# Kernel tuning notes

Measured on AMD Instinct MI355X. Metric: run time of the kernel, lower is better.

Reference implementation:

```python
import jax, jax.numpy as jnp
import numpy as np

T, B, E, H = 1024, 4, 1024, 16


def setup_inputs() -> dict:
    key0 = jax.random.key(0)
    ks = jax.random.split(key0, 10)
    query = jax.random.normal(ks[0], (T, B, E), jnp.float32)
    key_t = jax.random.normal(ks[1], (T, B, E), jnp.float32)
    # causal additive mask [T, T] (0 on/below diagonal, -inf above)
    causal = jnp.where(jnp.tril(jnp.ones((T, T), bool)), 0.0, -jnp.inf).astype(jnp.float32)
    # per-row valid lengths in [T//2, T]; True = padded key position
    lengths = jax.random.randint(ks[2], (B,), T // 2, T + 1)
    key_padding_mask = jnp.arange(T)[None, :] >= lengths[:, None]  # [B, T] bool
    scale = E ** -0.5
    Wq = jax.random.normal(ks[3], (E, E), jnp.float32) * scale
    Wk = jax.random.normal(ks[4], (E, E), jnp.float32) * scale
    Wv = jax.random.normal(ks[5], (E, E), jnp.float32) * scale
    bq = jax.random.normal(ks[6], (E,), jnp.float32) * 0.02
    bk = jax.random.normal(ks[7], (E,), jnp.float32) * 0.02
    bv = jax.random.normal(ks[8], (E,), jnp.float32) * 0.02
    return dict(query=query, key=key_t, key_padding_mask=key_padding_mask,
                attn_mask=causal, Wq=Wq, bq=bq, Wk=Wk, bk=bk, Wv=Wv, bv=bv,
                num_heads=H)


def reference(query, key, key_padding_mask, attn_mask, Wq, bq, Wk, bk, Wv, bv, num_heads):
    # Self-attention path (encoder_decoder_attention=False, layer_state=None):
    # k, v computed from `query`; `key` is unused (matches torch forward).
    t, b, e = query.shape
    h = num_heads
    d = e // h
    scaling = d ** -0.5
    q = (query @ Wq.T + bq) * scaling          # [T, B, E]
    k = query @ Wk.T + bk
    v = query @ Wv.T + bv

    def _shape(x):  # [T, B, E] -> [B*H, T, D]
        return x.reshape(t, b * h, d).transpose(1, 0, 2)

    q, k, v = _shape(q), _shape(k), _shape(v)
    attn = jnp.einsum('ztd,zsd->zts', q, k)    # [B*H, T, S]
    attn = attn.reshape(b, h, t, t) + attn_mask            # additive causal mask
    attn = jnp.where(key_padding_mask[:, None, None, :], -jnp.inf, attn)
    probs = jax.nn.softmax(attn, axis=-1)                   # dropout p=0.0
    out = jnp.einsum('bhts,bhsd->bhtd', probs, v.reshape(b, h, t, d))
    # [B,H,T,D] -> [B*H,T,D] -> [T,B*H,D] -> [T,B,E]
    out = out.reshape(b * h, t, d).transpose(1, 0, 2).reshape(t, b, e)
    return out
```

## Files before the change

kernel.cpp:

```cpp
#include <hip/hip_runtime.h>
#include <cstdint>


typedef __attribute__((ext_vector_type(8))) short short8;
typedef __attribute__((ext_vector_type(4))) float floatx4;
typedef __attribute__((ext_vector_type(16))) float floatx16;
typedef __attribute__((ext_vector_type(4))) unsigned short u16x4;
typedef unsigned short u16;

#define T_DIM 1024
#define B_DIM 4
#define E_DIM 1024
#define H_DIM 16
#define D_DIM 64
#define M_DIM (T_DIM * B_DIM)
#define N_DIM (3 * E_DIM)
#define K_DIM E_DIM
#define KT_NUM (K_DIM / 64)

__device__ __forceinline__ u16 f2bf(float f) {
  uint32_t u = __builtin_bit_cast(uint32_t, f);
  u += 0x7fffu + ((u >> 16) & 1u);
  return (u16)(u >> 16);
}

__device__ __forceinline__ void gload_lds16(const void* g, void* l) {
  __builtin_amdgcn_global_load_lds(
      (const __attribute__((address_space(1))) uint32_t*)g,
      (__attribute__((address_space(3))) uint32_t*)l, 16, 0, 0);
}

__device__ __forceinline__ uint32_t swz(uint32_t row, uint32_t cb) {
  return row * 128u + (cb ^ ((row & 7u) << 4));
}

#define BARRIER()  __builtin_amdgcn_s_barrier()
#define WAIT_VM6   asm volatile("s_waitcnt vmcnt(6)" ::: "memory")
#define WAIT_VM0   asm volatile("s_waitcnt vmcnt(0)" ::: "memory")

__global__ __launch_bounds__(256) void convert_k(
    const float* __restrict__ q, const float* __restrict__ wq,
    const float* __restrict__ wk, const float* __restrict__ wv,
    u16* __restrict__ Abf, u16* __restrict__ Wbf,
    const int* __restrict__ kpm, int* __restrict__ lengths) {
  if (blockIdx.x >= 7168) {
    __shared__ int cnt;
    if (threadIdx.x == 0) cnt = 0;
    __syncthreads();
    int b = blockIdx.x - 7168;
    int local = 0;
    for (int t = threadIdx.x; t < T_DIM; t += 256)
      local += (kpm[b * T_DIM + t] == 0) ? 1 : 0;
    atomicAdd(&cnt, local);
    __syncthreads();
    if (threadIdx.x == 0) lengths[b] = cnt;
    return;
  }
  size_t i = ((size_t)blockIdx.x * 256 + threadIdx.x) * 4;
  const float* src;
  u16* dst;
  if (i < (size_t)M_DIM * K_DIM) {
    src = q + i;
    dst = Abf + i;
  } else {
    size_t off = i - (size_t)M_DIM * K_DIM;
    int x = (int)(off >> 20);
    size_t within = off & 1048575u;
    src = (x == 0 ? wq : (x == 1 ? wk : wv)) + within;
    dst = Wbf + off;
  }
  float4 v = *(const float4*)src;
  u16x4 o;
  o.x = f2bf(v.x); o.y = f2bf(v.y); o.z = f2bf(v.z); o.w = f2bf(v.w);
  *(u16x4*)dst = o;
}

__global__ __launch_bounds__(512, 2) void qkv_gemm(
    const u16* __restrict__ A, const u16* __restrict__ W,
    const float* __restrict__ bq, const float* __restrict__ bk,
    const float* __restrict__ bv,
    u16* __restrict__ qo, u16* __restrict__ ko, u16* __restrict__ vto) {
  __shared__ alignas(16) char lds[131072];
  const int tid = threadIdx.x;
  const int lane = tid & 63, w = tid >> 6;
  const int fr = lane & 15, fg = lane >> 4;
  const int wm = (w >> 2) * 128, wn = (w & 3) * 64;
  const int srow = lane >> 3;
  const int scol = ((lane & 7) ^ srow) * 16;

  const int bid = blockIdx.x;
  const int sw = (bid & 7) * 24 + (bid >> 3);
  const int m0 = (sw / 12) * 256, n0 = (sw % 12) * 256;

  const char* A0 = lds;
  const char* B0 = lds + 32768;
  const char* A1 = lds + 65536;
  const char* B1 = lds + 98304;

  floatx4 acc[8][4] = {};
  short8 af[4][2];
  short8 bfr[4][2];

  auto stage = [&](int kt, int g) {
    if (kt >= KT_NUM) return;
    const bool isA = (g <= 1);
    const u16* src = isA ? A : W;
    const int base = isA
        ? ((w >> 2) * 128 + (g == 1 ? 64 : 0) + (w & 3) * 16)
        : ((w & 3) * 64 + (g == 3 ? 32 : 0) + (w >> 2) * 16);
    char* dstbuf = lds + (kt & 1) * 65536 + (isA ? 0 : 32768);
#pragma unroll
    for (int it = 0; it < 2; ++it) {
      int r = base + it * 8 + srow;
      int grow = isA ? (((m0 + r) & 1023) * 4 + ((m0 + r) >> 10)) : (n0 + r);
      gload_lds16((const char*)src + (size_t)grow * 2048 + kt * 128 + scol,
                  dstbuf + r * 128);
    }
  };
  auto read_a4 = [&](const char* ab, int rbase) {
#pragma unroll
    for (int i = 0; i < 4; ++i)
#pragma unroll
      for (int kk = 0; kk < 2; ++kk)
        af[i][kk] = *(const short8*)(ab + swz(rbase + i * 16 + fr, kk * 64 + fg * 16));
  };
  auto read_b2 = [&](const char* bb, int j0) {
#pragma unroll
    for (int j = 0; j < 2; ++j)
#pragma unroll
      for (int kk = 0; kk < 2; ++kk)
        bfr[j0 + j][kk] = *(const short8*)(bb + swz(wn + (j0 + j) * 16 + fr, kk * 64 + fg * 16));
  };
  auto mfma_quad = [&](int i0, int j0) {
    __builtin_amdgcn_s_setprio(1);
#pragma unroll
    for (int kk = 0; kk < 2; ++kk)
#pragma unroll
      for (int i = 0; i < 4; ++i)
#pragma unroll
        for (int j = 0; j < 2; ++j)
          acc[i0 + i][j0 + j] = __builtin_amdgcn_mfma_f32_16x16x32_bf16(
              af[i][kk], bfr[j0 + j][kk], acc[i0 + i][j0 + j], 0, 0, 0);
    __builtin_amdgcn_s_setprio(0);
  };

  stage(0, 0); stage(0, 1); stage(0, 2); stage(0, 3);
  stage(1, 0); stage(1, 2); stage(1, 3);
  WAIT_VM6;
  BARRIER();

  for (int i = 0; i < KT_NUM / 2; ++i) {
    const int t = 2 * i;
    const bool last = (i == KT_NUM / 2 - 1);
    read_a4(A0, wm);
    read_b2(B0, 0);
    stage(t + 1, 1);
    BARRIER();
    mfma_quad(0, 0);
    BARRIER();
    read_b2(B0, 2);
    stage(t + 2, 0);
    BARRIER();
    mfma_quad(0, 2);
    BARRIER();
    read_a4(A0, wm + 64);
    stage(t + 2, 2);
    BARRIER();
    mfma_quad(4, 2);
    BARRIER();
    stage(t + 2, 3);
    BARRIER();
    mfma_quad(4, 0);
    if (last) { WAIT_VM0; } else { WAIT_VM6; }
    BARRIER();
    read_a4(A1, wm);
    read_b2(B1, 0);
    stage(t + 2, 1);
    BARRIER();
    mfma_quad(0, 0);
    BARRIER();
    read_b2(B1, 2);
    stage(t + 3, 0);
    BARRIER();
    mfma_quad(0, 2);
    BARRIER();
    read_a4(A1, wm + 64);
    stage(t + 3, 2);
    BARRIER();
    mfma_quad(4, 2);
    BARRIER();
    stage(t + 3, 3);
    BARRIER();
    mfma_quad(4, 0);
    if (!last) WAIT_VM6;
    BARRIER();
  }

#pragma unroll
  for (int j = 0; j < 4; ++j) {
    int col = n0 + wn + j * 16 + fr;
    int x = col >> 10;
    int within = col & 1023;
    int h = within >> 6, d = within & 63;
    float bias = (x == 0) ? bq[within] : ((x == 1) ? bk[within] : bv[within]);
    float scale = (x == 0) ? 0.125f * 1.44269504f : 1.0f;
#pragma unroll
    for (int i = 0; i < 8; ++i) {
      int mp = m0 + wm + i * 16 + fg * 4;
      int b = mp >> 10, t0 = mp & 1023;
      int z = b * H_DIM + h;
      if (x == 2) {
        u16x4 pk;
#pragma unroll
        for (int r = 0; r < 4; ++r)
          pk[r] = f2bf(acc[i][j][r] + bias);
        *(u16x4*)(vto + (size_t)(z * D_DIM + d) * T_DIM + t0) = pk;
      } else {
        u16* dstp = (x == 0) ? qo : ko;
#pragma unroll
        for (int r = 0; r < 4; ++r)
          dstp[((size_t)z * T_DIM + t0 + r) * D_DIM + d] =
              f2bf((acc[i][j][r] + bias) * scale);
      }
    }
  }
}

__global__ __launch_bounds__(256) void attn_k(
    const u16* __restrict__ qbuf, const u16* __restrict__ kbuf,
    const u16* __restrict__ vtb, const int* __restrict__ lengths,
    float* __restrict__ out) {
  __shared__ alignas(16) char Klds[2][64 * 128];
  __shared__ alignas(16) char Vlds[2][64 * 128];

  const int bid = blockIdx.x;
  const int swzid = (bid & 7) * 64 + (bid >> 3);
  const int z = swzid >> 3;
  const int qb = 7 - (swzid & 7);
  const int b = z >> 4, h = z & 15;
  const int tid = threadIdx.x, lane = tid & 63, w = tid >> 6;
  const int l31 = lane & 31, hi = lane >> 5;
  const int srow = lane >> 3;
  const int scol = ((lane & 7) ^ srow) * 16;

  const int length = lengths[b];
  const int t0 = qb * 128;
  const int t0w = t0 + w * 32;
  const int t = t0w + l31;
  const int s_hi = min(t0 + 128, length);
  const int n_tiles = (s_hi + 63) >> 6;

  short8 qf[4];
#pragma unroll
  for (int dk = 0; dk < 4; ++dk)
    qf[dk] = *(const short8*)(qbuf + ((size_t)z * T_DIM + t) * D_DIM + dk * 16 + hi * 8);

  floatx16 accT[2] = {};
  float m = -1e30f, lsum = 0.f;

  auto stageKV = [&](int st, int buf) {
    const int s0 = st * 64;
#pragma unroll
    for (int it = 0; it < 2; ++it) {
      int rb = w * 16 + it * 8;
      gload_lds16((const char*)kbuf + ((size_t)z * T_DIM + s0 + rb + srow) * 128 + scol,
                  Klds[buf] + rb * 128);
      gload_lds16((const char*)vtb + ((size_t)(z * D_DIM + rb + srow)) * 2048 + s0 * 2 + scol,
                  Vlds[buf] + rb * 128);
    }
  };

  stageKV(0, 0);
  __syncthreads();
  int cur = 0;

  for (int st = 0; st < n_tiles; ++st) {
    const int s0 = st * 64;
    if (st + 1 < n_tiles) stageKV(st + 1, cur ^ 1);

    if (s0 <= t0w + 31) {
      floatx16 sT[2] = {};
      __builtin_amdgcn_s_setprio(1);
#pragma unroll
      for (int sh = 0; sh < 2; ++sh)
#pragma unroll
        for (int dk = 0; dk < 4; ++dk) {
          short8 kf = *(const short8*)(Klds[cur] + swz(sh * 32 + l31, dk * 32 + hi * 16));
          sT[sh] = __builtin_amdgcn_mfma_f32_32x32x16_bf16(kf, qf[dk], sT[sh], 0, 0, 0);
        }
      __builtin_amdgcn_s_setprio(0);

      if (s0 + 63 > t0w || s0 + 63 >= length) {
#pragma unroll
        for (int sh = 0; sh < 2; ++sh)
#pragma unroll
          for (int r = 0; r < 16; ++r) {
            int s = s0 + sh * 32 + (r & 3) + 8 * (r >> 2) + 4 * hi;
            if (s > t || s >= length) sT[sh][r] = -1e30f;
          }
      }

      float tmax = -1e30f;
#pragma unroll
      for (int sh = 0; sh < 2; ++sh)
#pragma unroll
        for (int r = 0; r < 16; ++r) tmax = fmaxf(tmax, sT[sh][r]);
      tmax = fmaxf(tmax, __shfl_xor(tmax, 32, 64));
      if (!__all(tmax <= m + 8.0f)) {
        float mn = fmaxf(m, tmax);
        float corr = __builtin_exp2f(m - mn);
        m = mn;
        lsum *= corr;
#pragma unroll
        for (int dh = 0; dh < 2; ++dh)
#pragma unroll
          for (int r = 0; r < 16; ++r) accT[dh][r] *= corr;
      }
      float rs = 0.f;
#pragma unroll
      for (int sh = 0; sh < 2; ++sh)
#pragma unroll
        for (int r = 0; r < 16; ++r) {
          float p = __builtin_exp2f(sT[sh][r] - m);
          sT[sh][r] = p;
          rs += p;
        }
      lsum += rs;

#pragma unroll
      for (int sh = 0; sh < 2; ++sh) {
        uint32_t a[8];
#pragma unroll
        for (int i = 0; i < 8; ++i)
          asm("v_cvt_pk_bf16_f32 %0, %1, %2"
              : "=v"(a[i]) : "v"(sT[sh][2 * i]), "v"(sT[sh][2 * i + 1]));
        uint32_t oth[8];
#pragma unroll
        for (int i = 0; i < 8; ++i)
          oth[i] = (uint32_t)__shfl_xor((int)a[i], 32, 64);
        short8 pa[2];
#pragma unroll
        for (int q = 0; q < 2; ++q) {
          union { uint32_t u[4]; short8 v; } pk;
          pk.u[0] = hi ? oth[4 * q + 2] : a[4 * q + 0];
          pk.u[1] = hi ? oth[4 * q + 3] : a[4 * q + 1];
          pk.u[2] = hi ? a[4 * q + 2] : oth[4 * q + 0];
          pk.u[3] = hi ? a[4 * q + 3] : oth[4 * q + 1];
          pa[q] = pk.v;
        }
        __builtin_amdgcn_s_setprio(1);
#pragma unroll
        for (int dh = 0; dh < 2; ++dh)
#pragma unroll
          for (int q = 0; q < 2; ++q) {
            int ks = sh * 2 + q;
            short8 vf = *(const short8*)(Vlds[cur] + swz(dh * 32 + l31, ks * 32 + hi * 16));
            accT[dh] = __builtin_amdgcn_mfma_f32_32x32x16_bf16(vf, pa[q], accT[dh], 0, 0, 0);
          }
        __builtin_amdgcn_s_setprio(0);
      }
    }

    __syncthreads();
    cur ^= 1;
  }

  lsum += __shfl_xor(lsum, 32, 64);
  float inv = 1.0f / lsum;
#pragma unroll
  for (int dh = 0; dh < 2; ++dh)
#pragma unroll
    for (int q = 0; q < 4; ++q) {
      float4 o4;
      o4.x = accT[dh][4 * q + 0] * inv;
      o4.y = accT[dh][4 * q + 1] * inv;
      o4.z = accT[dh][4 * q + 2] * inv;
      o4.w = accT[dh][4 * q + 3] * inv;
      int d = 8 * q + 4 * hi + 32 * dh;
      *(float4*)(out + (size_t)t * (B_DIM * E_DIM) + b * E_DIM + h * D_DIM + d) = o4;
    }
}

extern "C" void kernel_launch(void* const* d_in, const int* in_sizes, int n_in,
                              void* d_out, int out_size, void* d_ws, size_t ws_size,
                              hipStream_t stream) {
  const float* query = (const float*)d_in[0];
  const int* kpm = (const int*)d_in[2];
  const float* Wq = (const float*)d_in[4];
  const float* bq = (const float*)d_in[5];
  const float* Wk = (const float*)d_in[6];
  const float* bk = (const float*)d_in[7];
  const float* Wv = (const float*)d_in[8];
  const float* bv = (const float*)d_in[9];

  char* ws = (char*)d_ws;
  u16* Abf = (u16*)ws;
  u16* Wbf = (u16*)(ws + 8388608);
  u16* qb_ = (u16*)(ws + 14680064);
  u16* kb_ = (u16*)(ws + 23068672);
  u16* vtb = (u16*)(ws + 31457280);
  int* lengths = (int*)(ws + 39845888);

  convert_k<<<7172, 256, 0, stream>>>(query, Wq, Wk, Wv, Abf, Wbf, kpm, lengths);
  qkv_gemm<<<192, 512, 0, stream>>>(Abf, Wbf, bq, bk, bv, qb_, kb_, vtb);
  attn_k<<<512, 256, 0, stream>>>(qb_, kb_, vtb, lengths, (float*)d_out);
}
```

Measured before the change: 94.59 us.

## Retile QKV GEMM to 128x384 blocks with 256 workgroups

Changes the QKV projection GEMM tile from 256x256 to 128x384 per workgroup, so the grid grows from 192 to 256 blocks and fills the 256 CUs of the MI355X. Each wave now computes a 64x96 sub-tile with a 4x6 accumulator array, and the staging and MFMA schedule are rewritten around three B column pairs. The aim is to remove the partial-wave imbalance of 192 blocks, at the cost of lower arithmetic intensity per tile and more global reads of A.

```diff
diff --git a/kernel.cpp b/kernel.cpp
--- a/kernel.cpp
+++ b/kernel.cpp
@@ -84,120 +84,119 @@
   const int tid = threadIdx.x;
   const int lane = tid & 63, w = tid >> 6;
   const int fr = lane & 15, fg = lane >> 4;
-  const int wm = (w >> 2) * 128, wn = (w & 3) * 64;
+  const int wm = (w >> 2) * 64, wn = (w & 3) * 96;
   const int srow = lane >> 3;
   const int scol = ((lane & 7) ^ srow) * 16;
 
   const int bid = blockIdx.x;
-  const int sw = (bid & 7) * 24 + (bid >> 3);
-  const int m0 = (sw / 12) * 256, n0 = (sw % 12) * 256;
-
-  const char* A0 = lds;
-  const char* B0 = lds + 32768;
-  const char* A1 = lds + 65536;
-  const char* B1 = lds + 98304;
-
-  floatx4 acc[8][4] = {};
+  const int n0 = (bid & 7) * 384;
+  const int m0 = (bid >> 3) * 128;
+
+  floatx4 acc[4][6] = {};
   short8 af[4][2];
-  short8 bfr[4][2];
+  short8 bfr[6][2];
 
   auto stage = [&](int kt, int g) {
     if (kt >= KT_NUM) return;
-    const bool isA = (g <= 1);
-    const u16* src = isA ? A : W;
-    const int base = isA
-        ? ((w >> 2) * 128 + (g == 1 ? 64 : 0) + (w & 3) * 16)
-        : ((w & 3) * 64 + (g == 3 ? 32 : 0) + (w >> 2) * 16);
-    char* dstbuf = lds + (kt & 1) * 65536 + (isA ? 0 : 32768);
+    char* buf = lds + (kt & 1) * 65536;
 #pragma unroll
     for (int it = 0; it < 2; ++it) {
-      int r = base + it * 8 + srow;
-      int grow = isA ? (((m0 + r) & 1023) * 4 + ((m0 + r) >> 10)) : (n0 + r);
-      gload_lds16((const char*)src + (size_t)grow * 2048 + kt * 128 + scol,
-                  dstbuf + r * 128);
+      int mrow = it * 64 + w * 8 + srow;
+      if (g == 0) {
+        int gr = m0 + mrow;
+        int ga = (gr & 1023) * 4 + (gr >> 10);
+        gload_lds16((const char*)A + (size_t)ga * 2048 + kt * 128 + scol,
+                    buf + mrow * 128);
+      } else {
+        int r = 16 * (3 * (mrow >> 4) + (g - 1)) + (mrow & 15);
+        gload_lds16((const char*)W + (size_t)(n0 + r) * 2048 + kt * 128 + scol,
+                    buf + 16384 + r * 128);
+      }
     }
   };
-  auto read_a4 = [&](const char* ab, int rbase) {
+  auto read_a = [&](const char* buf) {
 #pragma unroll
     for (int i = 0; i < 4; ++i)
 #pragma unroll
       for (int kk = 0; kk < 2; ++kk)
-        af[i][kk] = *(const short8*)(ab + swz(rbase + i * 16 + fr, kk * 64 + fg * 16));
+        af[i][kk] = *(const short8*)(buf + swz(wm + i * 16 + fr, kk * 64 + fg * 16));
   };
-  auto read_b2 = [&](const char* bb, int j0) {
-#pragma unroll
-    for (int j = 0; j < 2; ++j)
+  auto read_b = [&](const char* buf, int j0) {
+#pragma unroll
+    for (int jj = 0; jj < 2; ++jj) {
+      int j = j0 + jj * 3;
 #pragma unroll
       for (int kk = 0; kk < 2; ++kk)
-        bfr[j0 + j][kk] = *(const short8*)(bb + swz(wn + (j0 + j) * 16 + fr, kk * 64 + fg * 16));
+        bfr[j][kk] = *(const short8*)(buf + 16384 +
+                                      swz(wn + j * 16 + fr, kk * 64 + fg * 16));
+    }
   };
-  auto mfma_quad = [&](int i0, int j0) {
+  auto mfma_pair = [&](int j0) {
     __builtin_amdgcn_s_setprio(1);
 #pragma unroll
     for (int kk = 0; kk < 2; ++kk)
 #pragma unroll
       for (int i = 0; i < 4; ++i)
 #pragma unroll
-        for (int j = 0; j < 2; ++j)
-          acc[i0 + i][j0 + j] = __builtin_amdgcn_mfma_f32_16x16x32_bf16(
-              af[i][kk], bfr[j0 + j][kk], acc[i0 + i][j0 + j], 0, 0, 0);
+        for (int jj = 0; jj < 2; ++jj) {
+          int j = j0 + jj * 3;
+          acc[i][j] = __builtin_amdgcn_mfma_f32_16x16x32_bf16(
+              af[i][kk], bfr[j][kk], acc[i][j], 0, 0, 0);
+        }
     __builtin_amdgcn_s_setprio(0);
   };
 
   stage(0, 0); stage(0, 1); stage(0, 2); stage(0, 3);
-  stage(1, 0); stage(1, 2); stage(1, 3);
+  stage(1, 0); stage(1, 1); stage(1, 2);
   WAIT_VM6;
   BARRIER();
+
+  const char* buf0 = lds;
+  const char* buf1 = lds + 65536;
 
   for (int i = 0; i < KT_NUM / 2; ++i) {
     const int t = 2 * i;
     const bool last = (i == KT_NUM / 2 - 1);
-    read_a4(A0, wm);
-    read_b2(B0, 0);
-    stage(t + 1, 1);
-    BARRIER();
-    mfma_quad(0, 0);
-    BARRIER();
-    read_b2(B0, 2);
+    read_a(buf0);
+    read_b(buf0, 0);
+    stage(t + 1, 3);
+    BARRIER();
+    mfma_pair(0);
+    BARRIER();
+    read_b(buf0, 1);
     stage(t + 2, 0);
-    BARRIER();
-    mfma_quad(0, 2);
-    BARRIER();
-    read_a4(A0, wm + 64);
+    stage(t + 2, 1);
+    BARRIER();
+    mfma_pair(1);
+    BARRIER();
+    read_b(buf0, 2);
     stage(t + 2, 2);
     BARRIER();
-    mfma_quad(4, 2);
-    BARRIER();
+    mfma_pair(2);
+    if (last) { WAIT_VM0; } else { WAIT_VM6; }
+    BARRIER();
+    read_a(buf1);
+    read_b(buf1, 0);
     stage(t + 2, 3);
     BARRIER();
-    mfma_quad(4, 0);
-    if (last) { WAIT_VM0; } else { WAIT_VM6; }
-    BARRIER();
-    read_a4(A1, wm);
-    read_b2(B1, 0);
-    stage(t + 2, 1);
-    BARRIER();
-    mfma_quad(0, 0);
-    BARRIER();
-    read_b2(B1, 2);
+    mfma_pair(0);
+    BARRIER();
+    read_b(buf1, 1);
     stage(t + 3, 0);
-    BARRIER();
-    mfma_quad(0, 2);
-    BARRIER();
-    read_a4(A1, wm + 64);
+    stage(t + 3, 1);
+    BARRIER();
+    mfma_pair(1);
+    BARRIER();
+    read_b(buf1, 2);
     stage(t + 3, 2);
     BARRIER();
-    mfma_quad(4, 2);
-    BARRIER();
-    stage(t + 3, 3);
-    BARRIER();
-    mfma_quad(4, 0);
+    mfma_pair(2);
     if (!last) WAIT_VM6;
     BARRIER();
   }
 
 #pragma unroll
-  for (int j = 0; j < 4; ++j) {
+  for (int j = 0; j < 6; ++j) {
     int col = n0 + wn + j * 16 + fr;
     int x = col >> 10;
     int within = col & 1023;
@@ -205,7 +204,7 @@
     float bias = (x == 0) ? bq[within] : ((x == 1) ? bk[within] : bv[within]);
     float scale = (x == 0) ? 0.125f * 1.44269504f : 1.0f;
 #pragma unroll
-    for (int i = 0; i < 8; ++i) {
+    for (int i = 0; i < 4; ++i) {
       int mp = m0 + wm + i * 16 + fg * 4;
       int b = mp >> 10, t0 = mp & 1023;
       int z = b * H_DIM + h;
@@ -402,6 +401,6 @@
   int* lengths = (int*)(ws + 39845888);
 
   convert_k<<<7172, 256, 0, stream>>>(query, Wq, Wk, Wv, Abf, Wbf, kpm, lengths);
-  qkv_gemm<<<192, 512, 0, stream>>>(Abf, Wbf, bq, bk, bv, qb_, kb_, vtb);
+  qkv_gemm<<<256, 512, 0, stream>>>(Abf, Wbf, bq, bk, bv, qb_, kb_, vtb);
   attn_k<<<512, 256, 0, stream>>>(qb_, kb_, vtb, lengths, (float*)d_out);
 }
```

Measured after the change: 85.64 us. 1.1x faster.
